# Optimization experiments

Measured on AMD Instinct MI355X. Metric: run time of the kernel, lower is better.

Reference implementation:

```python
import jax, jax.numpy as jnp
import numpy as np

HEADS = 8


def setup_inputs() -> dict:
    key = jax.random.key(0)
    k1, k2, k3, k4, k5, k6 = jax.random.split(key, 6)
    B, S, E = 2, 2048, 512
    D = E // HEADS
    return {
        "values": jax.random.normal(k1, (B, S, E), dtype=jnp.float32),
        "keys": jax.random.normal(k2, (B, S, E), dtype=jnp.float32),
        "queries": jax.random.normal(k3, (B, S, E), dtype=jnp.float32),
        "mask": jax.random.randint(k4, (B, 1, 1, S), 0, 2, dtype=jnp.int32),
        "W_v": jax.random.normal(k5, (D, D), dtype=jnp.float32) * (1.0 / np.sqrt(D)),
        "W_o": jax.random.normal(k6, (E, E), dtype=jnp.float32) * (1.0 / np.sqrt(E)),
        "b_o": jnp.zeros((E,), dtype=jnp.float32),
    }


def reference(values, keys, queries, mask, W_v, W_o, b_o):
    B, S, E = queries.shape
    H = HEADS
    D = E // H
    # reshape to (b, s, h, d) and apply the SAME W_v linear to v, k, q
    # (faithful to the original, which calls self.values on all three)
    v = jnp.einsum('bshd,ed->bshe', values.reshape(B, -1, H, D), W_v)
    k = jnp.einsum('bshd,ed->bshe', keys.reshape(B, -1, H, D), W_v)
    q = jnp.einsum('bshd,ed->bshe', queries.reshape(B, -1, H, D), W_v)
    # unscaled attention scores (original has no 1/sqrt(d))
    energy = jnp.einsum('bqhd,bkhd->bhqk', q, k)  # (b, h, q, k)
    energy = jnp.where(mask == 0, -jnp.inf, energy)
    attn = jax.nn.softmax(energy, axis=3)
    out = jnp.einsum('bhqk,bkhd->bqhd', attn, v)  # (b, q, h, d)
    out = out.reshape(B, S, E)
    return out @ W_o.T + b_o
```

## Files before the change

kernel.cpp:

```cpp
#include <hip/hip_runtime.h>


#define B_ 2
#define S_ 2048
#define E_ 512
#define H_ 8
#define D_ 64

typedef unsigned short ushort_t;
typedef __attribute__((ext_vector_type(8))) short short8;
typedef __attribute__((ext_vector_type(8))) _Float16 half8;
typedef __attribute__((ext_vector_type(4))) float f32x4;

__device__ __forceinline__ ushort_t f2bs(float x) {
    union { float f; unsigned int u; } a; a.f = x;
    unsigned int u = a.u;
    u += 0x7fffu + ((u >> 16) & 1u);
    return (ushort_t)(u >> 16);
}
__device__ __forceinline__ float bs2f(ushort_t h) {
    union { unsigned int u; float f; } a; a.u = ((unsigned int)h) << 16;
    return a.f;
}
__device__ __forceinline__ ushort_t f2hs(float x) {
    _Float16 h = (_Float16)x;
    ushort_t u; __builtin_memcpy(&u, &h, 2);
    return u;
}
__device__ __forceinline__ void split16(const float4* g, ushort_t* hi, ushort_t* lo) {
    #pragma unroll
    for (int q = 0; q < 4; ++q) {
        float4 f = g[q];
        float vv[4] = {f.x, f.y, f.z, f.w};
        #pragma unroll
        for (int j = 0; j < 4; ++j) {
            ushort_t h = f2bs(vv[j]);
            hi[q * 4 + j] = h;
            lo[q * 4 + j] = f2bs(vv[j] - bs2f(h));
        }
    }
}

__global__ void __launch_bounds__(256) proj_mfma(
    const float* __restrict__ quer, const float* __restrict__ keys,
    const float* __restrict__ vals, const float* __restrict__ Wv,
    ushort_t* __restrict__ qf, ushort_t* __restrict__ kf,
    ushort_t* __restrict__ vt)
{
    __shared__ ushort_t Ah[64 * 72], Al[64 * 72];
    __shared__ ushort_t Bh[64 * 72], Bl[64 * 72];
    const int tens = blockIdx.y;
    const float* src = tens == 0 ? quer : (tens == 1 ? keys : vals);
    const int bx = blockIdx.x;
    const int st = bx & 31, bh = bx >> 5;
    const int b = bh >> 3, h = bh & 7;
    const int s0 = st * 64;
    const int t = threadIdx.x;

    {
        int e = t >> 2, dg = (t & 3) * 16;
        ushort_t th[16], tl[16];
        split16((const float4*)(Wv + e * 64 + dg), th, tl);
        *(uint4*)&Bh[e * 72 + dg] = *(uint4*)th;  *(uint4*)&Bh[e * 72 + dg + 8] = *(uint4*)(th + 8);
        *(uint4*)&Bl[e * 72 + dg] = *(uint4*)tl;  *(uint4*)&Bl[e * 72 + dg + 8] = *(uint4*)(tl + 8);
    }
    {
        int row = t >> 2, cg = (t & 3) * 16;
        const float* g = src + ((size_t)b * S_ + s0 + row) * 512 + h * 64 + cg;
        ushort_t th[16], tl[16];
        split16((const float4*)g, th, tl);
        *(uint4*)&Ah[row * 72 + cg] = *(uint4*)th;  *(uint4*)&Ah[row * 72 + cg + 8] = *(uint4*)(th + 8);
        *(uint4*)&Al[row * 72 + cg] = *(uint4*)tl;  *(uint4*)&Al[row * 72 + cg + 8] = *(uint4*)(tl + 8);
    }
    __syncthreads();

    const int w = t >> 6, lm = t & 15, quad = (t >> 4) & 3;
    f32x4 acc[4];
    #pragma unroll
    for (int nt = 0; nt < 4; ++nt) acc[nt] = (f32x4){0.f, 0.f, 0.f, 0.f};

    #pragma unroll
    for (int kk = 0; kk < 2; ++kk) {
        short8 ah = *(const short8*)&Ah[(w * 16 + lm) * 72 + kk * 32 + quad * 8];
        short8 al = *(const short8*)&Al[(w * 16 + lm) * 72 + kk * 32 + quad * 8];
        #pragma unroll
        for (int nt = 0; nt < 4; ++nt) {
            short8 bh8 = *(const short8*)&Bh[(nt * 16 + lm) * 72 + kk * 32 + quad * 8];
            short8 bl8 = *(const short8*)&Bl[(nt * 16 + lm) * 72 + kk * 32 + quad * 8];
            acc[nt] = __builtin_amdgcn_mfma_f32_16x16x32_bf16(ah, bh8, acc[nt], 0, 0, 0);
            acc[nt] = __builtin_amdgcn_mfma_f32_16x16x32_bf16(al, bh8, acc[nt], 0, 0, 0);
            acc[nt] = __builtin_amdgcn_mfma_f32_16x16x32_bf16(ah, bl8, acc[nt], 0, 0, 0);
        }
    }

    if (tens < 2) {
        ushort_t* dst = tens == 0 ? qf : kf;
        #pragma unroll
        for (int nt = 0; nt < 4; ++nt) {
            #pragma unroll
            for (int r = 0; r < 4; ++r) {
                size_t addr = ((size_t)bh * S_ + s0 + w * 16 + quad * 4 + r) * 64 + nt * 16 + lm;
                dst[addr] = f2hs(acc[nt][r]);
            }
        }
    } else {
        #pragma unroll
        for (int nt = 0; nt < 4; ++nt) {
            unsigned int p0 = (unsigned int)f2bs(acc[nt][0]) | ((unsigned int)f2bs(acc[nt][1]) << 16);
            unsigned int p1 = (unsigned int)f2bs(acc[nt][2]) | ((unsigned int)f2bs(acc[nt][3]) << 16);
            uint2 pk; pk.x = p0; pk.y = p1;
            size_t addr = ((size_t)bh * 64 + nt * 16 + lm) * S_ + s0 + w * 16 + quad * 4;
            *(uint2*)&vt[addr] = pk;
        }
    }
}

__global__ void __launch_bounds__(256) attn_mfma(
    const ushort_t* __restrict__ qf, const ushort_t* __restrict__ kf,
    const ushort_t* __restrict__ vt, const int* __restrict__ mask,
    ushort_t* __restrict__ ctx)
{
    __shared__ ushort_t Ks[64 * 72];
    __shared__ ushort_t Vt[64 * 72];
    __shared__ ushort_t Ps[4 * 16 * 72];
    __shared__ float    mbias[64];

    const int bx = blockIdx.x;
    const int qt = bx & 31;
    const int bh = bx >> 5;
    const int b  = bh >> 3, h = bh & 7;
    const int t  = threadIdx.x;
    const int w = t >> 6, lm = t & 15, quad = (t >> 4) & 3;
    const int q0 = qt * 64;
    const int wbase = w * 16 * 72;

    half8 aq[2];
    {
        size_t qrow = ((size_t)bh * S_ + q0 + w * 16 + lm) * 64 + quad * 8;
        #pragma unroll
        for (int kk = 0; kk < 2; ++kk)
            aq[kk] = *(const half8*)&qf[qrow + kk * 32];
    }
    short8 ones;
    #pragma unroll
    for (int j = 0; j < 8; ++j) ones[j] = (short)0x3F80;

    f32x4 acc[4];
    #pragma unroll
    for (int nt = 0; nt < 4; ++nt) acc[nt] = (f32x4){0.f, 0.f, 0.f, 0.f};
    f32x4 acc_l = (f32x4){0.f, 0.f, 0.f, 0.f};

    for (int kc = 0; kc < S_ / 64; ++kc) {
        __syncthreads();
        {
            int row = t >> 2, cg = (t & 3) * 16;
            size_t gaddr = ((size_t)bh * S_ + kc * 64 + row) * 64 + cg;
            *(uint4*)&Ks[row * 72 + cg]     = *(const uint4*)&kf[gaddr];
            *(uint4*)&Ks[row * 72 + cg + 8] = *(const uint4*)&kf[gaddr + 8];
        }
        {
            int row = t >> 2, cg = (t & 3) * 16;
            size_t gaddr = ((size_t)bh * 64 + row) * S_ + kc * 64 + cg;
            *(uint4*)&Vt[row * 72 + cg]     = *(const uint4*)&vt[gaddr];
            *(uint4*)&Vt[row * 72 + cg + 8] = *(const uint4*)&vt[gaddr + 8];
        }
        if (t < 64) mbias[t] = mask[b * S_ + kc * 64 + t] ? -64.f : -1e30f;
        __syncthreads();

        #pragma unroll
        for (int nt = 0; nt < 4; ++nt) {
            f32x4 s = (f32x4){0.f, 0.f, 0.f, 0.f};
            #pragma unroll
            for (int kk = 0; kk < 2; ++kk) {
                half8 bk = *(const half8*)&Ks[(nt * 16 + lm) * 72 + kk * 32 + quad * 8];
                s = __builtin_amdgcn_mfma_f32_16x16x32_f16(aq[kk], bk, s, 0, 0, 0);
            }
            float mv = mbias[nt * 16 + lm];
            #pragma unroll
            for (int r = 0; r < 4; ++r) {
                float p = __expf(s[r] + mv);
                Ps[wbase + (quad * 4 + r) * 72 + nt * 16 + lm] = f2bs(p);
            }
        }
        __builtin_amdgcn_s_waitcnt(0);

        #pragma unroll
        for (int kk = 0; kk < 2; ++kk) {
            short8 ap = *(const short8*)&Ps[wbase + lm * 72 + kk * 32 + quad * 8];
            #pragma unroll
            for (int nt = 0; nt < 4; ++nt) {
                short8 bv = *(const short8*)&Vt[(nt * 16 + lm) * 72 + kk * 32 + quad * 8];
                acc[nt] = __builtin_amdgcn_mfma_f32_16x16x32_bf16(ap, bv, acc[nt], 0, 0, 0);
            }
            acc_l = __builtin_amdgcn_mfma_f32_16x16x32_bf16(ap, ones, acc_l, 0, 0, 0);
        }
    }

    #pragma unroll
    for (int r = 0; r < 4; ++r) {
        float inv = 1.f / acc_l[r];
        int s = q0 + w * 16 + quad * 4 + r;
        #pragma unroll
        for (int nt = 0; nt < 4; ++nt) {
            int d = nt * 16 + lm;
            ctx[((size_t)b * S_ + s) * E_ + h * D_ + d] = f2bs(acc[nt][r] * inv);
        }
    }
}

__global__ void __launch_bounds__(256) outproj_mfma(
    const ushort_t* __restrict__ ctx, const float* __restrict__ Wo,
    const float* __restrict__ bo, float* __restrict__ out)
{
    __shared__ ushort_t As[64 * 72];
    __shared__ ushort_t Bs[64 * 72];
    const int m0 = blockIdx.x * 64, n0 = blockIdx.y * 64;
    const int t = threadIdx.x;
    const int w = t >> 6, lm = t & 15, quad = (t >> 4) & 3;

    f32x4 acc[4];
    #pragma unroll
    for (int nt = 0; nt < 4; ++nt) acc[nt] = (f32x4){0.f, 0.f, 0.f, 0.f};

    for (int kc = 0; kc < E_ / 64; ++kc) {
        __syncthreads();
        {
            int row = t >> 2, cg = (t & 3) * 16;
            const ushort_t* g = ctx + (size_t)(m0 + row) * E_ + kc * 64 + cg;
            *(uint4*)&As[row * 72 + cg]     = *(const uint4*)g;
            *(uint4*)&As[row * 72 + cg + 8] = *(const uint4*)(g + 8);
        }
        {
            int n = t >> 2, kg = (t & 3) * 16;
            const float4* g = (const float4*)(Wo + (size_t)(n0 + n) * E_ + kc * 64 + kg);
            ushort_t tmp[16];
            #pragma unroll
            for (int q = 0; q < 4; ++q) {
                float4 f = g[q];
                tmp[q * 4 + 0] = f2bs(f.x); tmp[q * 4 + 1] = f2bs(f.y);
                tmp[q * 4 + 2] = f2bs(f.z); tmp[q * 4 + 3] = f2bs(f.w);
            }
            *(uint4*)&Bs[n * 72 + kg]     = *(uint4*)tmp;
            *(uint4*)&Bs[n * 72 + kg + 8] = *(uint4*)(tmp + 8);
        }
        __syncthreads();

        #pragma unroll
        for (int kk = 0; kk < 2; ++kk) {
            short8 a = *(const short8*)&As[(w * 16 + lm) * 72 + kk * 32 + quad * 8];
            #pragma unroll
            for (int nt = 0; nt < 4; ++nt) {
                short8 bb = *(const short8*)&Bs[(nt * 16 + lm) * 72 + kk * 32 + quad * 8];
                acc[nt] = __builtin_amdgcn_mfma_f32_16x16x32_bf16(a, bb, acc[nt], 0, 0, 0);
            }
        }
    }

    #pragma unroll
    for (int nt = 0; nt < 4; ++nt) {
        float bias = bo[n0 + nt * 16 + lm];
        #pragma unroll
        for (int r = 0; r < 4; ++r) {
            int m = m0 + w * 16 + quad * 4 + r;
            out[(size_t)m * E_ + n0 + nt * 16 + lm] = acc[nt][r] + bias;
        }
    }
}

extern "C" void kernel_launch(void* const* d_in, const int* in_sizes, int n_in,
                              void* d_out, int out_size, void* d_ws, size_t ws_size,
                              hipStream_t stream) {
    const float* vals = (const float*)d_in[0];
    const float* keys = (const float*)d_in[1];
    const float* quer = (const float*)d_in[2];
    const int*   mask = (const int*)d_in[3];
    const float* Wv   = (const float*)d_in[4];
    const float* Wo   = (const float*)d_in[5];
    const float* bo   = (const float*)d_in[6];
    float* out = (float*)d_out;

    const size_t N = (size_t)B_ * H_ * S_ * D_;
    ushort_t* ws  = (ushort_t*)d_ws;
    ushort_t* qf  = ws;
    ushort_t* kf  = ws + N;
    ushort_t* vt  = ws + 2 * N;
    ushort_t* ctx = ws + 3 * N;

    proj_mfma<<<dim3(B_ * H_ * (S_ / 64), 3), 256, 0, stream>>>(
        quer, keys, vals, Wv, qf, kf, vt);
    attn_mfma<<<B_ * H_ * (S_ / 64), 256, 0, stream>>>(qf, kf, vt, mask, ctx);
    outproj_mfma<<<dim3((B_ * S_) / 64, E_ / 64), 256, 0, stream>>>(ctx, Wo, bo, out);
}
```

Baseline: 147.8 us.

## Process 128-key chunks and compute transposed scores for vectorized P stores

The attention kernel now loads 128 keys per iteration instead of 64, which halves the number of barrier-synchronized loop trips. QK^T is computed with K as the A operand, so each lane holds 4 consecutive keys for one query and writes P as one packed 8-byte store instead of four scalar stores. The mask is read straight from global memory as an int4 rather than staged through shared memory, and the shared-memory strides are widened for the larger tiles. The cost is more LDS per block and per-lane global mask loads inside the inner loop, which may reduce occupancy.

```diff
diff --git a/kernel.cpp b/kernel.cpp
--- a/kernel.cpp
+++ b/kernel.cpp
@@ -96,13 +96,12 @@
     if (tens < 2) {
         ushort_t* dst = tens == 0 ? qf : kf;
         #pragma unroll
-        for (int nt = 0; nt < 4; ++nt) {
+        for (int nt = 0; nt < 4; ++nt)
             #pragma unroll
             for (int r = 0; r < 4; ++r) {
                 size_t addr = ((size_t)bh * S_ + s0 + w * 16 + quad * 4 + r) * 64 + nt * 16 + lm;
                 dst[addr] = f2hs(acc[nt][r]);
             }
-        }
     } else {
         #pragma unroll
         for (int nt = 0; nt < 4; ++nt) {
@@ -115,15 +114,17 @@
     }
 }
 
+#define KSTR 72
+#define VSTR 136
+#define PSTR 136
 __global__ void __launch_bounds__(256) attn_mfma(
     const ushort_t* __restrict__ qf, const ushort_t* __restrict__ kf,
     const ushort_t* __restrict__ vt, const int* __restrict__ mask,
     ushort_t* __restrict__ ctx)
 {
-    __shared__ ushort_t Ks[64 * 72];
-    __shared__ ushort_t Vt[64 * 72];
-    __shared__ ushort_t Ps[4 * 16 * 72];
-    __shared__ float    mbias[64];
+    __shared__ ushort_t Ks[128 * KSTR];
+    __shared__ ushort_t Vt[64 * VSTR];
+    __shared__ ushort_t Ps[4][16 * PSTR];
 
     const int bx = blockIdx.x;
     const int qt = bx & 31;
@@ -132,7 +133,6 @@
     const int t  = threadIdx.x;
     const int w = t >> 6, lm = t & 15, quad = (t >> 4) & 3;
     const int q0 = qt * 64;
-    const int wbase = w * 16 * 72;
 
     half8 aq[2];
     {
@@ -150,46 +150,52 @@
     for (int nt = 0; nt < 4; ++nt) acc[nt] = (f32x4){0.f, 0.f, 0.f, 0.f};
     f32x4 acc_l = (f32x4){0.f, 0.f, 0.f, 0.f};
 
-    for (int kc = 0; kc < S_ / 64; ++kc) {
-        __syncthreads();
-        {
-            int row = t >> 2, cg = (t & 3) * 16;
-            size_t gaddr = ((size_t)bh * S_ + kc * 64 + row) * 64 + cg;
-            *(uint4*)&Ks[row * 72 + cg]     = *(const uint4*)&kf[gaddr];
-            *(uint4*)&Ks[row * 72 + cg + 8] = *(const uint4*)&kf[gaddr + 8];
-        }
-        {
-            int row = t >> 2, cg = (t & 3) * 16;
-            size_t gaddr = ((size_t)bh * 64 + row) * S_ + kc * 64 + cg;
-            *(uint4*)&Vt[row * 72 + cg]     = *(const uint4*)&vt[gaddr];
-            *(uint4*)&Vt[row * 72 + cg + 8] = *(const uint4*)&vt[gaddr + 8];
-        }
-        if (t < 64) mbias[t] = mask[b * S_ + kc * 64 + t] ? -64.f : -1e30f;
-        __syncthreads();
-
-        #pragma unroll
-        for (int nt = 0; nt < 4; ++nt) {
+    for (int kc = 0; kc < S_ / 128; ++kc) {
+        __syncthreads();
+        {
+            int row = t >> 1, cg = (t & 1) * 32;
+            const ushort_t* g = &kf[((size_t)bh * S_ + kc * 128 + row) * 64 + cg];
+            ushort_t* d = &Ks[row * KSTR + cg];
+            *(uint4*)&d[0]  = *(const uint4*)&g[0];
+            *(uint4*)&d[8]  = *(const uint4*)&g[8];
+            *(uint4*)&d[16] = *(const uint4*)&g[16];
+            *(uint4*)&d[24] = *(const uint4*)&g[24];
+        }
+        {
+            int row = t >> 2, cg = (t & 3) * 32;
+            const ushort_t* g = &vt[((size_t)bh * 64 + row) * S_ + kc * 128 + cg];
+            ushort_t* d = &Vt[row * VSTR + cg];
+            *(uint4*)&d[0]  = *(const uint4*)&g[0];
+            *(uint4*)&d[8]  = *(const uint4*)&g[8];
+            *(uint4*)&d[16] = *(const uint4*)&g[16];
+            *(uint4*)&d[24] = *(const uint4*)&g[24];
+        }
+        __syncthreads();
+
+        #pragma unroll
+        for (int mt = 0; mt < 8; ++mt) {
             f32x4 s = (f32x4){0.f, 0.f, 0.f, 0.f};
             #pragma unroll
             for (int kk = 0; kk < 2; ++kk) {
-                half8 bk = *(const half8*)&Ks[(nt * 16 + lm) * 72 + kk * 32 + quad * 8];
-                s = __builtin_amdgcn_mfma_f32_16x16x32_f16(aq[kk], bk, s, 0, 0, 0);
-            }
-            float mv = mbias[nt * 16 + lm];
-            #pragma unroll
-            for (int r = 0; r < 4; ++r) {
-                float p = __expf(s[r] + mv);
-                Ps[wbase + (quad * 4 + r) * 72 + nt * 16 + lm] = f2bs(p);
-            }
-        }
-        __builtin_amdgcn_s_waitcnt(0);
-
-        #pragma unroll
-        for (int kk = 0; kk < 2; ++kk) {
-            short8 ap = *(const short8*)&Ps[wbase + lm * 72 + kk * 32 + quad * 8];
+                half8 ak = *(const half8*)&Ks[(mt * 16 + lm) * KSTR + kk * 32 + quad * 8];
+                s = __builtin_amdgcn_mfma_f32_16x16x32_f16(ak, aq[kk], s, 0, 0, 0);
+            }
+            int4 mi = *(const int4*)&mask[b * S_ + kc * 128 + mt * 16 + quad * 4];
+            ushort_t p4[4];
+            p4[0] = f2bs(__expf(s[0] + (mi.x ? -64.f : -1e30f)));
+            p4[1] = f2bs(__expf(s[1] + (mi.y ? -64.f : -1e30f)));
+            p4[2] = f2bs(__expf(s[2] + (mi.z ? -64.f : -1e30f)));
+            p4[3] = f2bs(__expf(s[3] + (mi.w ? -64.f : -1e30f)));
+            *(uint2*)&Ps[w][lm * PSTR + mt * 16 + quad * 4] = *(uint2*)p4;
+        }
+        __asm__ volatile("s_waitcnt lgkmcnt(0)" ::: "memory");
+
+        #pragma unroll
+        for (int kk = 0; kk < 4; ++kk) {
+            short8 ap = *(const short8*)&Ps[w][lm * PSTR + kk * 32 + quad * 8];
             #pragma unroll
             for (int nt = 0; nt < 4; ++nt) {
-                short8 bv = *(const short8*)&Vt[(nt * 16 + lm) * 72 + kk * 32 + quad * 8];
+                short8 bv = *(const short8*)&Vt[(nt * 16 + lm) * VSTR + kk * 32 + quad * 8];
                 acc[nt] = __builtin_amdgcn_mfma_f32_16x16x32_bf16(ap, bv, acc[nt], 0, 0, 0);
             }
             acc_l = __builtin_amdgcn_mfma_f32_16x16x32_bf16(ap, ones, acc_l, 0, 0, 0);
```

Measured after the change: 175.7 us. +18.8%, slower.

## Rewrite attention kernel with 32x32 MFMA tiles, 2 waves, register prefetch

Applied to the files above, without the earlier changes.

The attention kernel now runs with 2 waves of 128 threads per block, each wave handling 32 query rows with 32x32x16 MFMA instructions computing S^T (K as the A operand, Q as B). The next K/V tile is prefetched into registers while the current tile is being computed. The row sum is accumulated in scalar registers instead of through an extra MFMA against a ones vector, and the mask is read directly from global memory. This cuts LDS traffic and MFMA instruction count per tile. The trade-off is fewer waves per block, which lowers occupancy and latency hiding, and more register pressure from the prefetch buffers.

```diff
diff --git a/kernel.cpp b/kernel.cpp
--- a/kernel.cpp
+++ b/kernel.cpp
@@ -11,12 +11,17 @@
 typedef __attribute__((ext_vector_type(8))) short short8;
 typedef __attribute__((ext_vector_type(8))) _Float16 half8;
 typedef __attribute__((ext_vector_type(4))) float f32x4;
+typedef __attribute__((ext_vector_type(16))) float f32x16;
 
 __device__ __forceinline__ ushort_t f2bs(float x) {
     union { float f; unsigned int u; } a; a.f = x;
     unsigned int u = a.u;
     u += 0x7fffu + ((u >> 16) & 1u);
     return (ushort_t)(u >> 16);
+}
+__device__ __forceinline__ ushort_t f2bs_fast(float x) {
+    union { float f; unsigned int u; } a; a.f = x;
+    return (ushort_t)((a.u + 0x8000u) >> 16);
 }
 __device__ __forceinline__ float bs2f(ushort_t h) {
     union { unsigned int u; float f; } a; a.u = ((unsigned int)h) << 16;
@@ -96,13 +101,12 @@
     if (tens < 2) {
         ushort_t* dst = tens == 0 ? qf : kf;
         #pragma unroll
-        for (int nt = 0; nt < 4; ++nt) {
+        for (int nt = 0; nt < 4; ++nt)
             #pragma unroll
             for (int r = 0; r < 4; ++r) {
                 size_t addr = ((size_t)bh * S_ + s0 + w * 16 + quad * 4 + r) * 64 + nt * 16 + lm;
                 dst[addr] = f2hs(acc[nt][r]);
             }
-        }
     } else {
         #pragma unroll
         for (int nt = 0; nt < 4; ++nt) {
@@ -115,95 +119,125 @@
     }
 }
 
-__global__ void __launch_bounds__(256) attn_mfma(
+#define KSTR 72
+#define VSTR 72
+#define PSTR 72
+__global__ void __launch_bounds__(128) attn_mfma(
     const ushort_t* __restrict__ qf, const ushort_t* __restrict__ kf,
     const ushort_t* __restrict__ vt, const int* __restrict__ mask,
     ushort_t* __restrict__ ctx)
 {
-    __shared__ ushort_t Ks[64 * 72];
-    __shared__ ushort_t Vt[64 * 72];
-    __shared__ ushort_t Ps[4 * 16 * 72];
-    __shared__ float    mbias[64];
+    __shared__ ushort_t Ks[64 * KSTR];
+    __shared__ ushort_t Vt[64 * VSTR];
+    __shared__ ushort_t Ps[2][32 * PSTR];
+    __shared__ float    linv[2][32];
 
     const int bx = blockIdx.x;
     const int qt = bx & 31;
     const int bh = bx >> 5;
-    const int b  = bh >> 3, h = bh & 7;
+    const int b  = bh >> 3, hd = bh & 7;
     const int t  = threadIdx.x;
-    const int w = t >> 6, lm = t & 15, quad = (t >> 4) & 3;
-    const int q0 = qt * 64;
-    const int wbase = w * 16 * 72;
-
-    half8 aq[2];
+    const int w  = t >> 6;
+    const int lane = t & 63;
+    const int lm = lane & 31;
+    const int hh = lane >> 5;
+    const int q0 = qt * 64 + w * 32;
+
+    half8 qfr[4];
     {
-        size_t qrow = ((size_t)bh * S_ + q0 + w * 16 + lm) * 64 + quad * 8;
-        #pragma unroll
-        for (int kk = 0; kk < 2; ++kk)
-            aq[kk] = *(const half8*)&qf[qrow + kk * 32];
-    }
-    short8 ones;
-    #pragma unroll
-    for (int j = 0; j < 8; ++j) ones[j] = (short)0x3F80;
-
-    f32x4 acc[4];
-    #pragma unroll
-    for (int nt = 0; nt < 4; ++nt) acc[nt] = (f32x4){0.f, 0.f, 0.f, 0.f};
-    f32x4 acc_l = (f32x4){0.f, 0.f, 0.f, 0.f};
-
-    for (int kc = 0; kc < S_ / 64; ++kc) {
+        size_t base = ((size_t)bh * S_ + q0 + lm) * 64 + hh * 8;
+        #pragma unroll
+        for (int ksl = 0; ksl < 4; ++ksl)
+            qfr[ksl] = *(const half8*)&qf[base + ksl * 16];
+    }
+
+    f32x16 acc[2];
+    #pragma unroll
+    for (int dt = 0; dt < 2; ++dt)
+        #pragma unroll
+        for (int i = 0; i < 16; ++i) acc[dt][i] = 0.f;
+    float ls = 0.f;
+
+    const int srow = t >> 1, scg = (t & 1) * 32;
+    const ushort_t* kg = &kf[((size_t)bh * S_ + srow) * 64 + scg];
+    const ushort_t* vg = &vt[((size_t)bh * 64 + srow) * S_ + scg];
+
+    uint4 kreg[4], vreg[4];
+    {
+        #pragma unroll
+        for (int j = 0; j < 4; ++j) {
+            kreg[j] = *(const uint4*)&kg[j * 8];
+            vreg[j] = *(const uint4*)&vg[j * 8];
+        }
+    }
+
+    for (int kc = 0; kc < 32; ++kc) {
         __syncthreads();
-        {
-            int row = t >> 2, cg = (t & 3) * 16;
-            size_t gaddr = ((size_t)bh * S_ + kc * 64 + row) * 64 + cg;
-            *(uint4*)&Ks[row * 72 + cg]     = *(const uint4*)&kf[gaddr];
-            *(uint4*)&Ks[row * 72 + cg + 8] = *(const uint4*)&kf[gaddr + 8];
-        }
-        {
-            int row = t >> 2, cg = (t & 3) * 16;
-            size_t gaddr = ((size_t)bh * 64 + row) * S_ + kc * 64 + cg;
-            *(uint4*)&Vt[row * 72 + cg]     = *(const uint4*)&vt[gaddr];
-            *(uint4*)&Vt[row * 72 + cg + 8] = *(const uint4*)&vt[gaddr + 8];
-        }
-        if (t < 64) mbias[t] = mask[b * S_ + kc * 64 + t] ? -64.f : -1e30f;
+        #pragma unroll
+        for (int j = 0; j < 4; ++j) {
+            *(uint4*)&Ks[srow * KSTR + scg + j * 8] = kreg[j];
+            *(uint4*)&Vt[srow * VSTR + scg + j * 8] = vreg[j];
+        }
         __syncthreads();
-
-        #pragma unroll
-        for (int nt = 0; nt < 4; ++nt) {
-            f32x4 s = (f32x4){0.f, 0.f, 0.f, 0.f};
-            #pragma unroll
-            for (int kk = 0; kk < 2; ++kk) {
-                half8 bk = *(const half8*)&Ks[(nt * 16 + lm) * 72 + kk * 32 + quad * 8];
-                s = __builtin_amdgcn_mfma_f32_16x16x32_f16(aq[kk], bk, s, 0, 0, 0);
-            }
-            float mv = mbias[nt * 16 + lm];
-            #pragma unroll
-            for (int r = 0; r < 4; ++r) {
-                float p = __expf(s[r] + mv);
-                Ps[wbase + (quad * 4 + r) * 72 + nt * 16 + lm] = f2bs(p);
-            }
-        }
-        __builtin_amdgcn_s_waitcnt(0);
-
-        #pragma unroll
-        for (int kk = 0; kk < 2; ++kk) {
-            short8 ap = *(const short8*)&Ps[wbase + lm * 72 + kk * 32 + quad * 8];
-            #pragma unroll
-            for (int nt = 0; nt < 4; ++nt) {
-                short8 bv = *(const short8*)&Vt[(nt * 16 + lm) * 72 + kk * 32 + quad * 8];
-                acc[nt] = __builtin_amdgcn_mfma_f32_16x16x32_bf16(ap, bv, acc[nt], 0, 0, 0);
-            }
-            acc_l = __builtin_amdgcn_mfma_f32_16x16x32_bf16(ap, ones, acc_l, 0, 0, 0);
-        }
-    }
-
-    #pragma unroll
-    for (int r = 0; r < 4; ++r) {
-        float inv = 1.f / acc_l[r];
-        int s = q0 + w * 16 + quad * 4 + r;
-        #pragma unroll
-        for (int nt = 0; nt < 4; ++nt) {
-            int d = nt * 16 + lm;
-            ctx[((size_t)b * S_ + s) * E_ + h * D_ + d] = f2bs(acc[nt][r] * inv);
+        if (kc + 1 < 32) {
+            const ushort_t* kp = kg + (size_t)(kc + 1) * 64 * 64;
+            const ushort_t* vp = vg + (size_t)(kc + 1) * 64;
+            #pragma unroll
+            for (int j = 0; j < 4; ++j) {
+                kreg[j] = *(const uint4*)&kp[j * 8];
+                vreg[j] = *(const uint4*)&vp[j * 8];
+            }
+        }
+
+        const int mbase = b * S_ + kc * 64;
+        #pragma unroll
+        for (int mt = 0; mt < 2; ++mt) {
+            f32x16 s;
+            #pragma unroll
+            for (int i = 0; i < 16; ++i) s[i] = 0.f;
+            #pragma unroll
+            for (int ksl = 0; ksl < 4; ++ksl) {
+                half8 ak = *(const half8*)&Ks[(mt * 32 + lm) * KSTR + ksl * 16 + hh * 8];
+                s = __builtin_amdgcn_mfma_f32_32x32x16_f16(ak, qfr[ksl], s, 0, 0, 0);
+            }
+            #pragma unroll
+            for (int g = 0; g < 4; ++g) {
+                int4 mi = *(const int4*)&mask[mbase + mt * 32 + g * 8 + hh * 4];
+                float p0 = __expf(s[g * 4 + 0] + (mi.x ? -64.f : -1e30f));
+                float p1 = __expf(s[g * 4 + 1] + (mi.y ? -64.f : -1e30f));
+                float p2 = __expf(s[g * 4 + 2] + (mi.z ? -64.f : -1e30f));
+                float p3 = __expf(s[g * 4 + 3] + (mi.w ? -64.f : -1e30f));
+                ls += (p0 + p1) + (p2 + p3);
+                ushort_t p4[4] = {f2bs_fast(p0), f2bs_fast(p1), f2bs_fast(p2), f2bs_fast(p3)};
+                *(uint2*)&Ps[w][lm * PSTR + mt * 32 + g * 8 + hh * 4] = *(uint2*)p4;
+            }
+        }
+        __asm__ volatile("s_waitcnt lgkmcnt(0)" ::: "memory");
+
+        #pragma unroll
+        for (int ksl = 0; ksl < 4; ++ksl) {
+            short8 ap = *(const short8*)&Ps[w][lm * PSTR + ksl * 16 + hh * 8];
+            #pragma unroll
+            for (int dt = 0; dt < 2; ++dt) {
+                short8 bv = *(const short8*)&Vt[(dt * 32 + lm) * VSTR + ksl * 16 + hh * 8];
+                acc[dt] = __builtin_amdgcn_mfma_f32_32x32x16_bf16(ap, bv, acc[dt], 0, 0, 0);
+            }
+        }
+    }
+
+    ls += __shfl_xor(ls, 32);
+    if (hh == 0) linv[w][lm] = 1.f / ls;
+    __asm__ volatile("s_waitcnt lgkmcnt(0)" ::: "memory");
+    float li[16];
+    #pragma unroll
+    for (int r = 0; r < 16; ++r) li[r] = linv[w][(r & 3) + 8 * (r >> 2) + 4 * hh];
+    #pragma unroll
+    for (int dt = 0; dt < 2; ++dt) {
+        #pragma unroll
+        for (int r = 0; r < 16; ++r) {
+            int s = q0 + (r & 3) + 8 * (r >> 2) + 4 * hh;
+            int d = dt * 32 + lm;
+            ctx[((size_t)b * S_ + s) * E_ + hd * D_ + d] = f2bs(acc[dt][r] * li[r]);
         }
     }
 }
@@ -288,6 +322,6 @@
 
     proj_mfma<<<dim3(B_ * H_ * (S_ / 64), 3), 256, 0, stream>>>(
         quer, keys, vals, Wv, qf, kf, vt);
-    attn_mfma<<<B_ * H_ * (S_ / 64), 256, 0, stream>>>(qf, kf, vt, mask, ctx);
+    attn_mfma<<<B_ * H_ * (S_ / 64), 128, 0, stream>>>(qf, kf, vt, mask, ctx);
     outproj_mfma<<<dim3((B_ * S_) / 64, E_ / 64), 256, 0, stream>>>(ctx, Wo, bo, out);
 }
```

Result: slower. 197.2 us (+33.4%).
